# Kernel tuning notes

Hardware: AMD Instinct MI355X
Metric: run time of the kernel (lower is better)

The kernel has to match this reference:

```python
import jax, jax.numpy as jnp
import numpy as np

IM_SIZE = (256, 256)
OVERSAMP = 1.25
WIDTH = 6
BETA = float(np.pi * np.sqrt((WIDTH / OVERSAMP * (OVERSAMP - 0.5)) ** 2 - 0.8))
OS_SIZE = tuple(int(np.ceil(OVERSAMP * n)) for n in IM_SIZE)  # (320, 320)
D = 2


def _kb(x):
    # Kaiser-Bessel interpolation kernel: i0(beta*sqrt(1-x^2)) for |x|<=1 (sigpy convention)
    return jnp.i0(BETA * jnp.sqrt(jnp.maximum(1.0 - x * x, 0.0)))


def setup_inputs() -> dict:
    key = jax.random.key(0)
    k1, k2, k3 = jax.random.split(key, 3)
    N, C = 1, 8
    img_r = jax.random.normal(k1, (N, C) + IM_SIZE, dtype=jnp.float32)
    img_i = jax.random.normal(k2, (N, C) + IM_SIZE, dtype=jnp.float32)
    # trajectory in [-N_i/2, N_i/2] per the class docstring
    trj = (jax.random.uniform(k3, (N, 64, 4096, D), dtype=jnp.float32) - 0.5) * 256.0
    return {"img_r": img_r, "img_i": img_i, "trj": trj}


def _nufft_forward(img_r, img_i, trj):
    img = (img_r + 1j * img_i).astype(jnp.complex64)  # (N, C, H, W)
    nd = img.ndim
    # --- apodization (inverse FT of KB kernel), separable per axis ---
    for a in range(D):
        n, osn = IM_SIZE[a], OS_SIZE[a]
        idx = jnp.arange(n, dtype=jnp.float32)
        arg = jnp.sqrt(BETA ** 2 - (np.pi * WIDTH * (idx - n // 2) / osn) ** 2)
        apod = arg / jnp.sinh(arg)
        shape = [1] * nd
        shape[nd - D + a] = n
        img = img * apod.reshape(shape)
    # --- scale + centered zero-pad to oversampled grid ---
    img = img / np.sqrt(float(np.prod(IM_SIZE)))
    pads = [(0, 0)] * (nd - D) + [(((o - n) // 2), (o - n) - ((o - n) // 2))
                                  for n, o in zip(IM_SIZE, OS_SIZE)]
    img = jnp.pad(img, pads)
    # --- centered FFT (ifftshift -> fftn(norm=None) -> fftshift) ---
    axes = tuple(range(-D, 0))
    ksp_os = jnp.fft.fftshift(jnp.fft.fftn(jnp.fft.ifftshift(img, axes=axes), axes=axes), axes=axes)
    # --- scale trajectory to oversampled grid coordinates ---
    scale = jnp.array([OS_SIZE[a] / IM_SIZE[a] for a in range(D)], jnp.float32)
    shift = jnp.array([OS_SIZE[a] // 2 for a in range(D)], jnp.float32)
    coord = trj * scale + shift  # (N, R, S, 2)
    x0 = jnp.ceil(coord - WIDTH / 2.0)
    # --- KB interpolation: fixed 6x6 neighbor loop, vectorized gather over all points ---
    N = img.shape[0]
    out = jnp.zeros((N,) + img.shape[1:nd - D] + coord.shape[1:-1], jnp.complex64)

    def gather(grid, ix, iy):  # grid (C, Hos, Wos), ix/iy (R, S) -> (C, R, S)
        return grid[:, ix, iy]

    for dx in range(WIDTH):
        px = x0[..., 0] + dx
        wx = _kb((px - coord[..., 0]) / (WIDTH / 2.0))
        ix = px.astype(jnp.int32) % OS_SIZE[0]
        for dy in range(WIDTH):
            py = x0[..., 1] + dy
            wy = _kb((py - coord[..., 1]) / (WIDTH / 2.0))
            iy = py.astype(jnp.int32) % OS_SIZE[1]
            vals = jax.vmap(gather)(ksp_os, ix, iy)  # (N, C, R, S)
            out = out + vals * (wx * wy)[:, None, :, :]
    return out / (WIDTH ** D)


def reference(img_r, img_i, trj):
    return _nufft_forward(img_r, img_i, trj)
```

## Files before the change

kernel.cpp:

```cpp
#include <hip/hip_runtime.h>
#include <math.h>

#define NCH   8
#define IMN   256
#define OSN   320
#define NPTS  (64*4096)
#define KD    512
#define BETA_F   10.9551078f
#define BETA2_F  120.014389f
#define APOD_C   0.05890486225f
#define GROWS 326
#define GCOLS 328
#define GPITCH (GCOLS * NCH)

typedef unsigned short u16;
typedef unsigned int   u32;
typedef __attribute__((ext_vector_type(8))) short s16x8;
typedef __attribute__((ext_vector_type(4))) float f32x4;
typedef __attribute__((ext_vector_type(2))) float f32x2;

__device__ __forceinline__ u32 f2bf(float f) {
    u32 u = __float_as_uint(f);
    return (u + 0x7FFFu + ((u >> 16) & 1u)) >> 16;
}

__device__ __forceinline__ s16x8 derive_b2(s16x8 b) {
    union { s16x8 v; u32 d[4]; } in, out;
    in.v = b;
    #pragma unroll
    for (int i = 0; i < 4; i++) {
        u32 v = in.d[i];
        out.d[i] = ((v >> 16) | (v << 16)) ^ 0x8000u;
    }
    return out.v;
}

__device__ __forceinline__ float i0f(float t) {
    if (t < 3.75f) {
        float y = t * t * (1.0f / 14.0625f);
        return 1.0f + y * (3.5156229f + y * (3.0899424f + y * (1.2067492f +
                     y * (0.2659732f + y * (0.0360768f + y * 0.0045813f)))));
    }
    float z = 3.75f / t;
    float p = 0.39894228f + z * (0.01328592f + z * (0.00225319f + z * (-0.00157565f +
              z * (0.00916281f + z * (-0.02057706f + z * (0.02635537f +
              z * (-0.01647633f + z * 0.00392377f)))))));
    return expf(t) * rsqrtf(t) * p;
}

__device__ __forceinline__ float apodf(int i) {
    float x = APOD_C * (float)(i - IMN / 2);
    float arg = sqrtf(BETA2_F - x * x);
    float e = expf(arg);
    float sh = 0.5f * (e - 1.0f / e);
    return arg / sh;
}

__global__ void prep(const float* __restrict__ r, const float* __restrict__ im,
                     u32* __restrict__ B1, u32* __restrict__ A) {
    const int b = blockIdx.x, t = threadIdx.x;
    if (b < (OSN * IMN) / 256) {
        int idx = b * 256 + t;
        int k = idx >> 8, j = idx & 255;
        int p = (k * (j + 32)) % OSN;
        float th = (2.0f * (float)M_PI / (float)OSN) * (float)p;
        float s = ((k + j) & 1) ? -1.0f : 1.0f;
        float sn, cs;
        sincosf(th, &sn, &cs);
        float re = s * cs, imv = -s * sn;
        B1[idx] = f2bf(re) | (f2bf(-imv) << 16);
    } else {
        int idx = (b - (OSN * IMN) / 256) * 256 + t;
        int i2 = idx & 255, i1 = (idx >> 8) & 255;
        float w = apodf(i1) * apodf(i2) * (1.0f / 256.0f);
        A[idx] = f2bf(r[idx] * w) | (f2bf(im[idx] * w) << 16);
    }
}

__launch_bounds__(64)
__global__ void gemm1(const short* __restrict__ Abf, const short* __restrict__ B1,
                      short* __restrict__ Tb) {
    const int c = blockIdx.z;
    const int mBase = blockIdx.y * 32;
    const int nBase = blockIdx.x * 32;
    const int t = threadIdx.x;
    const int fm = t & 15, fq = (t >> 4) * 8;
    const short* pa0  = Abf + (long)(c * IMN + mBase + fm) * KD + fq;
    const short* pa1  = pa0 + 16 * KD;
    const short* pb10 = B1 + (long)(nBase + fm) * KD + fq;
    const short* pb11 = pb10 + 16 * KD;
    f32x4 zz = {0.f, 0.f, 0.f, 0.f};
    f32x4 accRe[2][2], accIm[2][2];
    #pragma unroll
    for (int i = 0; i < 2; i++)
        #pragma unroll
        for (int j = 0; j < 2; j++) { accRe[i][j] = zz; accIm[i][j] = zz; }

    #pragma unroll
    for (int kc = 0; kc < 16; kc++) {
        const int kb = kc * 32;
        s16x8 a0  = *(const s16x8*)(pa0  + kb);
        s16x8 a1  = *(const s16x8*)(pa1  + kb);
        s16x8 b10 = *(const s16x8*)(pb10 + kb);
        s16x8 b11 = *(const s16x8*)(pb11 + kb);
        s16x8 b20 = derive_b2(b10);
        s16x8 b21 = derive_b2(b11);
        accRe[0][0] = __builtin_amdgcn_mfma_f32_16x16x32_bf16(a0, b10, accRe[0][0], 0, 0, 0);
        accRe[0][1] = __builtin_amdgcn_mfma_f32_16x16x32_bf16(a0, b11, accRe[0][1], 0, 0, 0);
        accRe[1][0] = __builtin_amdgcn_mfma_f32_16x16x32_bf16(a1, b10, accRe[1][0], 0, 0, 0);
        accRe[1][1] = __builtin_amdgcn_mfma_f32_16x16x32_bf16(a1, b11, accRe[1][1], 0, 0, 0);
        accIm[0][0] = __builtin_amdgcn_mfma_f32_16x16x32_bf16(a0, b20, accIm[0][0], 0, 0, 0);
        accIm[0][1] = __builtin_amdgcn_mfma_f32_16x16x32_bf16(a0, b21, accIm[0][1], 0, 0, 0);
        accIm[1][0] = __builtin_amdgcn_mfma_f32_16x16x32_bf16(a1, b20, accIm[1][0], 0, 0, 0);
        accIm[1][1] = __builtin_amdgcn_mfma_f32_16x16x32_bf16(a1, b21, accIm[1][1], 0, 0, 0);
    }
    #pragma unroll
    for (int i = 0; i < 2; i++)
        #pragma unroll
        for (int j = 0; j < 2; j++) {
            int i1b = mBase + i * 16 + (t >> 4) * 4;
            int k2  = nBase + j * 16 + fm;
            s16x8 v;
            #pragma unroll
            for (int r = 0; r < 4; r++) {
                v[2 * r]     = (short)f2bf(accRe[i][j][r]);
                v[2 * r + 1] = (short)f2bf(accIm[i][j][r]);
            }
            *(s16x8*)(Tb + ((long)(c * OSN + k2)) * KD + 2 * i1b) = v;
        }
}

__launch_bounds__(64)
__global__ void gemm2(const short* __restrict__ B1, const short* __restrict__ Tb,
                      u32* __restrict__ Gb) {
    const int c = blockIdx.z;
    const int mBase = blockIdx.y * 32;
    const int nBase = blockIdx.x * 32;
    const int t = threadIdx.x;
    const int fm = t & 15, fq = (t >> 4) * 8;
    const short* pa10 = B1 + (long)(mBase + fm) * KD + fq;
    const short* pa11 = pa10 + 16 * KD;
    const short* pb0  = Tb + ((long)(c * OSN + nBase + fm)) * KD + fq;
    const short* pb1  = pb0 + 16 * KD;
    f32x4 zz = {0.f, 0.f, 0.f, 0.f};
    f32x4 accRe[2][2], accIm[2][2];
    #pragma unroll
    for (int i = 0; i < 2; i++)
        #pragma unroll
        for (int j = 0; j < 2; j++) { accRe[i][j] = zz; accIm[i][j] = zz; }

    #pragma unroll
    for (int kc = 0; kc < 16; kc++) {
        const int kb = kc * 32;
        s16x8 a10 = *(const s16x8*)(pa10 + kb);
        s16x8 a11 = *(const s16x8*)(pa11 + kb);
        s16x8 b0  = *(const s16x8*)(pb0  + kb);
        s16x8 b1  = *(const s16x8*)(pb1  + kb);
        s16x8 a20 = derive_b2(a10);
        s16x8 a21 = derive_b2(a11);
        accRe[0][0] = __builtin_amdgcn_mfma_f32_16x16x32_bf16(a10, b0, accRe[0][0], 0, 0, 0);
        accRe[0][1] = __builtin_amdgcn_mfma_f32_16x16x32_bf16(a10, b1, accRe[0][1], 0, 0, 0);
        accRe[1][0] = __builtin_amdgcn_mfma_f32_16x16x32_bf16(a11, b0, accRe[1][0], 0, 0, 0);
        accRe[1][1] = __builtin_amdgcn_mfma_f32_16x16x32_bf16(a11, b1, accRe[1][1], 0, 0, 0);
        accIm[0][0] = __builtin_amdgcn_mfma_f32_16x16x32_bf16(a20, b0, accIm[0][0], 0, 0, 0);
        accIm[0][1] = __builtin_amdgcn_mfma_f32_16x16x32_bf16(a20, b1, accIm[0][1], 0, 0, 0);
        accIm[1][0] = __builtin_amdgcn_mfma_f32_16x16x32_bf16(a21, b0, accIm[1][0], 0, 0, 0);
        accIm[1][1] = __builtin_amdgcn_mfma_f32_16x16x32_bf16(a21, b1, accIm[1][1], 0, 0, 0);
    }
    #pragma unroll
    for (int i = 0; i < 2; i++)
        #pragma unroll
        for (int j = 0; j < 2; j++) {
            int k2 = nBase + j * 16 + fm;
            int pc  = k2 + 3;
            int pc2 = (k2 < 3) ? (k2 + 323) : ((k2 >= 317) ? (k2 - 317) : -1);
            #pragma unroll
            for (int r = 0; r < 4; r++) {
                int k1 = mBase + i * 16 + (t >> 4) * 4 + r;
                u32 val = f2bf(accRe[i][j][r]) | (f2bf(accIm[i][j][r]) << 16);
                int pr  = k1 + 3;
                int pr2 = (k1 < 3) ? (k1 + 323) : ((k1 >= 317) ? (k1 - 317) : -1);
                Gb[(long)pr * GPITCH + pc * NCH + c] = val;
                if (pr2 >= 0)              Gb[(long)pr2 * GPITCH + pc  * NCH + c] = val;
                if (pc2 >= 0)              Gb[(long)pr  * GPITCH + pc2 * NCH + c] = val;
                if (pr2 >= 0 && pc2 >= 0)  Gb[(long)pr2 * GPITCH + pc2 * NCH + c] = val;
            }
        }
}

__launch_bounds__(256, 4)
__global__ void interp_kernel(const float* __restrict__ trj,
                              const u32* __restrict__ grid,
                              u32* __restrict__ out) {
    const int t = threadIdx.x;
    __shared__ float wxs[64][6], wys[64][6];
    __shared__ int   x0s[64], y0s[64];

    if (t < 128) {
        int ptl = t & 63, axis = t >> 6;
        int pt = blockIdx.x * 64 + ptl;
        float tv = trj[pt * 2 + axis];
        float cc = __fadd_rn(__fmul_rn(tv, 1.25f), 160.0f);
        float v0 = ceilf(__fadd_rn(cc, -3.0f));
        if (axis) y0s[ptl] = (int)v0; else x0s[ptl] = (int)v0;
        float* ws = axis ? wys[ptl] : wxs[ptl];
        #pragma unroll
        for (int d = 0; d < 6; d++) {
            float u = __fdiv_rn(__fsub_rn(v0 + (float)d, cc), 3.0f);
            ws[d] = i0f(BETA_F * sqrtf(fmaxf(1.0f - u * u, 0.0f)));
        }
    }
    __syncthreads();

    const int pl = t >> 2;
    const int cp = (t & 3) * 2;
    const int px = x0s[pl] + 3;
    const int py = y0s[pl] + 3;
    const u32* g0 = grid + (long)px * GPITCH + py * NCH + cp;

    uint2 g[36];
    #pragma unroll
    for (int dx = 0; dx < 6; dx++)
        #pragma unroll
        for (int dy = 0; dy < 6; dy++)
            g[dx * 6 + dy] = *(const uint2*)(g0 + dx * GPITCH + dy * NCH);

    float wx[6], wy[6];
    #pragma unroll
    for (int d = 0; d < 6; d++) { wx[d] = wxs[pl][d]; wy[d] = wys[pl][d]; }

    float re0 = 0.f, im0 = 0.f, re1 = 0.f, im1 = 0.f;
    #pragma unroll
    for (int dx = 0; dx < 6; dx++) {
        float wxv = wx[dx];
        #pragma unroll
        for (int dy = 0; dy < 6; dy++) {
            uint2 gv = g[dx * 6 + dy];
            float ww = wxv * wy[dy];
            re0 += __uint_as_float(gv.x << 16) * ww;
            im0 += __uint_as_float(gv.x & 0xFFFF0000u) * ww;
            re1 += __uint_as_float(gv.y << 16) * ww;
            im1 += __uint_as_float(gv.y & 0xFFFF0000u) * ww;
        }
    }
    re0 *= (1.0f / 36.0f); im0 *= (1.0f / 36.0f);
    re1 *= (1.0f / 36.0f); im1 *= (1.0f / 36.0f);

    __shared__ float2 lds[64][9];
    lds[pl][cp]     = make_float2(re0, im0);
    lds[pl][cp + 1] = make_float2(re1, im1);
    __syncthreads();
    int c2 = t >> 5, p2 = t & 31;
    float2 va = lds[p2][c2];
    float2 vb = lds[p2 + 32][c2];
    long ob = (long)c2 * NPTS + blockIdx.x * 64;
    out[ob + p2]      = f2bf(va.y) | (f2bf(va.x) << 16);
    out[ob + p2 + 32] = f2bf(vb.y) | (f2bf(vb.x) << 16);
}

extern "C" void kernel_launch(void* const* d_in, const int* in_sizes, int n_in,
                              void* d_out, int out_size, void* d_ws, size_t ws_size,
                              hipStream_t stream) {
    const float* img_r = (const float*)d_in[0];
    const float* img_i = (const float*)d_in[1];
    const float* trj   = (const float*)d_in[2];

    char* ob = (char*)d_out;
    short* Tb  = (short*)(ob);
    u32*  B1u  = (u32*)(ob + 2621440);
    u32*  Au   = (u32*)(ob + 3276800);
    u32*  Gb   = (u32*)d_ws;

    prep<<<(OSN * IMN) / 256 + (NCH * IMN * IMN) / 256, 256, 0, stream>>>(
        img_r, img_i, B1u, Au);
    gemm1<<<dim3(OSN / 32, IMN / 32, NCH), 64, 0, stream>>>(
        (const short*)Au, (const short*)B1u, Tb);
    gemm2<<<dim3(OSN / 32, OSN / 32, NCH), 64, 0, stream>>>(
        (const short*)B1u, Tb, Gb);
    interp_kernel<<<NPTS / 64, 256, 0, stream>>>(trj, Gb, (u32*)d_out);
}
```

Before: 108.3 us.

## Halve GEMM tile N, spread interp weight computation, use packed f32x2 accumulation

Result: no change. 109.0 us (+0.6%).

```diff
diff --git a/kernel.cpp b/kernel.cpp
--- a/kernel.cpp
+++ b/kernel.cpp
@@ -82,19 +82,16 @@
                       short* __restrict__ Tb) {
     const int c = blockIdx.z;
     const int mBase = blockIdx.y * 32;
-    const int nBase = blockIdx.x * 32;
+    const int nBase = blockIdx.x * 16;
     const int t = threadIdx.x;
     const int fm = t & 15, fq = (t >> 4) * 8;
     const short* pa0  = Abf + (long)(c * IMN + mBase + fm) * KD + fq;
     const short* pa1  = pa0 + 16 * KD;
     const short* pb10 = B1 + (long)(nBase + fm) * KD + fq;
-    const short* pb11 = pb10 + 16 * KD;
     f32x4 zz = {0.f, 0.f, 0.f, 0.f};
-    f32x4 accRe[2][2], accIm[2][2];
-    #pragma unroll
-    for (int i = 0; i < 2; i++)
-        #pragma unroll
-        for (int j = 0; j < 2; j++) { accRe[i][j] = zz; accIm[i][j] = zz; }
+    f32x4 accRe[2], accIm[2];
+    #pragma unroll
+    for (int i = 0; i < 2; i++) { accRe[i] = zz; accIm[i] = zz; }
 
     #pragma unroll
     for (int kc = 0; kc < 16; kc++) {
@@ -102,32 +99,24 @@
         s16x8 a0  = *(const s16x8*)(pa0  + kb);
         s16x8 a1  = *(const s16x8*)(pa1  + kb);
         s16x8 b10 = *(const s16x8*)(pb10 + kb);
-        s16x8 b11 = *(const s16x8*)(pb11 + kb);
         s16x8 b20 = derive_b2(b10);
-        s16x8 b21 = derive_b2(b11);
-        accRe[0][0] = __builtin_amdgcn_mfma_f32_16x16x32_bf16(a0, b10, accRe[0][0], 0, 0, 0);
-        accRe[0][1] = __builtin_amdgcn_mfma_f32_16x16x32_bf16(a0, b11, accRe[0][1], 0, 0, 0);
-        accRe[1][0] = __builtin_amdgcn_mfma_f32_16x16x32_bf16(a1, b10, accRe[1][0], 0, 0, 0);
-        accRe[1][1] = __builtin_amdgcn_mfma_f32_16x16x32_bf16(a1, b11, accRe[1][1], 0, 0, 0);
-        accIm[0][0] = __builtin_amdgcn_mfma_f32_16x16x32_bf16(a0, b20, accIm[0][0], 0, 0, 0);
-        accIm[0][1] = __builtin_amdgcn_mfma_f32_16x16x32_bf16(a0, b21, accIm[0][1], 0, 0, 0);
-        accIm[1][0] = __builtin_amdgcn_mfma_f32_16x16x32_bf16(a1, b20, accIm[1][0], 0, 0, 0);
-        accIm[1][1] = __builtin_amdgcn_mfma_f32_16x16x32_bf16(a1, b21, accIm[1][1], 0, 0, 0);
-    }
-    #pragma unroll
-    for (int i = 0; i < 2; i++)
-        #pragma unroll
-        for (int j = 0; j < 2; j++) {
-            int i1b = mBase + i * 16 + (t >> 4) * 4;
-            int k2  = nBase + j * 16 + fm;
-            s16x8 v;
-            #pragma unroll
-            for (int r = 0; r < 4; r++) {
-                v[2 * r]     = (short)f2bf(accRe[i][j][r]);
-                v[2 * r + 1] = (short)f2bf(accIm[i][j][r]);
-            }
-            *(s16x8*)(Tb + ((long)(c * OSN + k2)) * KD + 2 * i1b) = v;
-        }
+        accRe[0] = __builtin_amdgcn_mfma_f32_16x16x32_bf16(a0, b10, accRe[0], 0, 0, 0);
+        accRe[1] = __builtin_amdgcn_mfma_f32_16x16x32_bf16(a1, b10, accRe[1], 0, 0, 0);
+        accIm[0] = __builtin_amdgcn_mfma_f32_16x16x32_bf16(a0, b20, accIm[0], 0, 0, 0);
+        accIm[1] = __builtin_amdgcn_mfma_f32_16x16x32_bf16(a1, b20, accIm[1], 0, 0, 0);
+    }
+    #pragma unroll
+    for (int i = 0; i < 2; i++) {
+        int i1b = mBase + i * 16 + (t >> 4) * 4;
+        int k2  = nBase + fm;
+        s16x8 v;
+        #pragma unroll
+        for (int r = 0; r < 4; r++) {
+            v[2 * r]     = (short)f2bf(accRe[i][r]);
+            v[2 * r + 1] = (short)f2bf(accIm[i][r]);
+        }
+        *(s16x8*)(Tb + ((long)(c * OSN + k2)) * KD + 2 * i1b) = v;
+    }
 }
 
 __launch_bounds__(64)
@@ -135,19 +124,16 @@
                       u32* __restrict__ Gb) {
     const int c = blockIdx.z;
     const int mBase = blockIdx.y * 32;
-    const int nBase = blockIdx.x * 32;
+    const int nBase = blockIdx.x * 16;
     const int t = threadIdx.x;
     const int fm = t & 15, fq = (t >> 4) * 8;
     const short* pa10 = B1 + (long)(mBase + fm) * KD + fq;
     const short* pa11 = pa10 + 16 * KD;
     const short* pb0  = Tb + ((long)(c * OSN + nBase + fm)) * KD + fq;
-    const short* pb1  = pb0 + 16 * KD;
     f32x4 zz = {0.f, 0.f, 0.f, 0.f};
-    f32x4 accRe[2][2], accIm[2][2];
-    #pragma unroll
-    for (int i = 0; i < 2; i++)
-        #pragma unroll
-        for (int j = 0; j < 2; j++) { accRe[i][j] = zz; accIm[i][j] = zz; }
+    f32x4 accRe[2], accIm[2];
+    #pragma unroll
+    for (int i = 0; i < 2; i++) { accRe[i] = zz; accIm[i] = zz; }
 
     #pragma unroll
     for (int kc = 0; kc < 16; kc++) {
@@ -155,37 +141,30 @@
         s16x8 a10 = *(const s16x8*)(pa10 + kb);
         s16x8 a11 = *(const s16x8*)(pa11 + kb);
         s16x8 b0  = *(const s16x8*)(pb0  + kb);
-        s16x8 b1  = *(const s16x8*)(pb1  + kb);
         s16x8 a20 = derive_b2(a10);
         s16x8 a21 = derive_b2(a11);
-        accRe[0][0] = __builtin_amdgcn_mfma_f32_16x16x32_bf16(a10, b0, accRe[0][0], 0, 0, 0);
-        accRe[0][1] = __builtin_amdgcn_mfma_f32_16x16x32_bf16(a10, b1, accRe[0][1], 0, 0, 0);
-        accRe[1][0] = __builtin_amdgcn_mfma_f32_16x16x32_bf16(a11, b0, accRe[1][0], 0, 0, 0);
-        accRe[1][1] = __builtin_amdgcn_mfma_f32_16x16x32_bf16(a11, b1, accRe[1][1], 0, 0, 0);
-        accIm[0][0] = __builtin_amdgcn_mfma_f32_16x16x32_bf16(a20, b0, accIm[0][0], 0, 0, 0);
-        accIm[0][1] = __builtin_amdgcn_mfma_f32_16x16x32_bf16(a20, b1, accIm[0][1], 0, 0, 0);
-        accIm[1][0] = __builtin_amdgcn_mfma_f32_16x16x32_bf16(a21, b0, accIm[1][0], 0, 0, 0);
-        accIm[1][1] = __builtin_amdgcn_mfma_f32_16x16x32_bf16(a21, b1, accIm[1][1], 0, 0, 0);
-    }
-    #pragma unroll
-    for (int i = 0; i < 2; i++)
-        #pragma unroll
-        for (int j = 0; j < 2; j++) {
-            int k2 = nBase + j * 16 + fm;
-            int pc  = k2 + 3;
-            int pc2 = (k2 < 3) ? (k2 + 323) : ((k2 >= 317) ? (k2 - 317) : -1);
-            #pragma unroll
-            for (int r = 0; r < 4; r++) {
-                int k1 = mBase + i * 16 + (t >> 4) * 4 + r;
-                u32 val = f2bf(accRe[i][j][r]) | (f2bf(accIm[i][j][r]) << 16);
-                int pr  = k1 + 3;
-                int pr2 = (k1 < 3) ? (k1 + 323) : ((k1 >= 317) ? (k1 - 317) : -1);
-                Gb[(long)pr * GPITCH + pc * NCH + c] = val;
-                if (pr2 >= 0)              Gb[(long)pr2 * GPITCH + pc  * NCH + c] = val;
-                if (pc2 >= 0)              Gb[(long)pr  * GPITCH + pc2 * NCH + c] = val;
-                if (pr2 >= 0 && pc2 >= 0)  Gb[(long)pr2 * GPITCH + pc2 * NCH + c] = val;
-            }
-        }
+        accRe[0] = __builtin_amdgcn_mfma_f32_16x16x32_bf16(a10, b0, accRe[0], 0, 0, 0);
+        accRe[1] = __builtin_amdgcn_mfma_f32_16x16x32_bf16(a11, b0, accRe[1], 0, 0, 0);
+        accIm[0] = __builtin_amdgcn_mfma_f32_16x16x32_bf16(a20, b0, accIm[0], 0, 0, 0);
+        accIm[1] = __builtin_amdgcn_mfma_f32_16x16x32_bf16(a21, b0, accIm[1], 0, 0, 0);
+    }
+    #pragma unroll
+    for (int i = 0; i < 2; i++) {
+        int k2 = nBase + fm;
+        int pc  = k2 + 3;
+        int pc2 = (k2 < 3) ? (k2 + 323) : ((k2 >= 317) ? (k2 - 317) : -1);
+        #pragma unroll
+        for (int r = 0; r < 4; r++) {
+            int k1 = mBase + i * 16 + (t >> 4) * 4 + r;
+            u32 val = f2bf(accRe[i][r]) | (f2bf(accIm[i][r]) << 16);
+            int pr  = k1 + 3;
+            int pr2 = (k1 < 3) ? (k1 + 323) : ((k1 >= 317) ? (k1 - 317) : -1);
+            Gb[(long)pr * GPITCH + pc * NCH + c] = val;
+            if (pr2 >= 0)              Gb[(long)pr2 * GPITCH + pc  * NCH + c] = val;
+            if (pc2 >= 0)              Gb[(long)pr  * GPITCH + pc2 * NCH + c] = val;
+            if (pr2 >= 0 && pc2 >= 0)  Gb[(long)pr2 * GPITCH + pc2 * NCH + c] = val;
+        }
+    }
 }
 
 __launch_bounds__(256, 4)
@@ -196,19 +175,23 @@
     __shared__ float wxs[64][6], wys[64][6];
     __shared__ int   x0s[64], y0s[64];
 
-    if (t < 128) {
-        int ptl = t & 63, axis = t >> 6;
+    #pragma unroll
+    for (int k = 0; k < 3; k++) {
+        int e = t + 256 * k;
+        int ptl = e / 12;
+        int rem = e - ptl * 12;
+        int axis = rem >= 6 ? 1 : 0;
+        int d = rem - axis * 6;
         int pt = blockIdx.x * 64 + ptl;
         float tv = trj[pt * 2 + axis];
         float cc = __fadd_rn(__fmul_rn(tv, 1.25f), 160.0f);
         float v0 = ceilf(__fadd_rn(cc, -3.0f));
-        if (axis) y0s[ptl] = (int)v0; else x0s[ptl] = (int)v0;
-        float* ws = axis ? wys[ptl] : wxs[ptl];
-        #pragma unroll
-        for (int d = 0; d < 6; d++) {
-            float u = __fdiv_rn(__fsub_rn(v0 + (float)d, cc), 3.0f);
-            ws[d] = i0f(BETA_F * sqrtf(fmaxf(1.0f - u * u, 0.0f)));
-        }
+        if (d == 0) {
+            if (axis) y0s[ptl] = (int)v0; else x0s[ptl] = (int)v0;
+        }
+        float u = __fdiv_rn(__fsub_rn(v0 + (float)d, cc), 3.0f);
+        float wv = i0f(BETA_F * sqrtf(fmaxf(1.0f - u * u, 0.0f)));
+        if (axis) wys[ptl][d] = wv; else wxs[ptl][d] = wv;
     }
     __syncthreads();
 
@@ -229,7 +212,7 @@
     #pragma unroll
     for (int d = 0; d < 6; d++) { wx[d] = wxs[pl][d]; wy[d] = wys[pl][d]; }
 
-    float re0 = 0.f, im0 = 0.f, re1 = 0.f, im1 = 0.f;
+    f32x2 a0 = {0.f, 0.f}, a1 = {0.f, 0.f};
     #pragma unroll
     for (int dx = 0; dx < 6; dx++) {
         float wxv = wx[dx];
@@ -237,18 +220,19 @@
         for (int dy = 0; dy < 6; dy++) {
             uint2 gv = g[dx * 6 + dy];
             float ww = wxv * wy[dy];
-            re0 += __uint_as_float(gv.x << 16) * ww;
-            im0 += __uint_as_float(gv.x & 0xFFFF0000u) * ww;
-            re1 += __uint_as_float(gv.y << 16) * ww;
-            im1 += __uint_as_float(gv.y & 0xFFFF0000u) * ww;
-        }
-    }
-    re0 *= (1.0f / 36.0f); im0 *= (1.0f / 36.0f);
-    re1 *= (1.0f / 36.0f); im1 *= (1.0f / 36.0f);
+            f32x2 w2 = {ww, ww};
+            f32x2 v0v = { __uint_as_float(gv.x << 16), __uint_as_float(gv.x & 0xFFFF0000u) };
+            f32x2 v1v = { __uint_as_float(gv.y << 16), __uint_as_float(gv.y & 0xFFFF0000u) };
+            a0 += v0v * w2;
+            a1 += v1v * w2;
+        }
+    }
+    f32x2 sc = {1.0f / 36.0f, 1.0f / 36.0f};
+    a0 *= sc; a1 *= sc;
 
     __shared__ float2 lds[64][9];
-    lds[pl][cp]     = make_float2(re0, im0);
-    lds[pl][cp + 1] = make_float2(re1, im1);
+    lds[pl][cp]     = make_float2(a0.x, a0.y);
+    lds[pl][cp + 1] = make_float2(a1.x, a1.y);
     __syncthreads();
     int c2 = t >> 5, p2 = t & 31;
     float2 va = lds[p2][c2];
@@ -273,9 +257,9 @@
 
     prep<<<(OSN * IMN) / 256 + (NCH * IMN * IMN) / 256, 256, 0, stream>>>(
         img_r, img_i, B1u, Au);
-    gemm1<<<dim3(OSN / 32, IMN / 32, NCH), 64, 0, stream>>>(
+    gemm1<<<dim3(OSN / 16, IMN / 32, NCH), 64, 0, stream>>>(
         (const short*)Au, (const short*)B1u, Tb);
-    gemm2<<<dim3(OSN / 32, OSN / 32, NCH), 64, 0, stream>>>(
+    gemm2<<<dim3(OSN / 16, OSN / 32, NCH), 64, 0, stream>>>(
         (const short*)B1u, Tb, Gb);
     interp_kernel<<<NPTS / 64, 256, 0, stream>>>(trj, Gb, (u32*)d_out);
 }
```
